# Kernel tuning notes

Hardware: AMD Instinct MI355X
Metric: run time of the kernel (lower is better)

Reference implementation:

```python
import jax, jax.numpy as jnp
import numpy as np

L = 10          # number of shooting steps
MU = 0.05       # mu hyperparameter
KS = 7          # gaussian kernel size
SIGMA = 2.0     # gaussian sigma
B, H, W = 16, 512, 512


def _conv2d(x, k, padding, groups=1):
    return jax.lax.conv_general_dilated(
        x, k, (1, 1), padding,
        dimension_numbers=('NCHW', 'OIHW', 'NCHW'),
        feature_group_count=groups)

# normalized sobel kernel (kornia SpatialGradient, abs-sum = 8)
_sobel_x = jnp.array([[-1., 0., 1.], [-2., 0., 2.], [-1., 0., 1.]], jnp.float32) / 8.0
_sobel_k = jnp.stack([_sobel_x, _sobel_x.T])[:, None]   # [2,1,3,3] -> dx, dy
_div_k = jnp.stack([_sobel_x, _sobel_x.T])[None]        # [1,2,3,3] divergence conv


def _gauss2d(ks, sigma):
    x = jnp.arange(ks, dtype=jnp.float32) - ks // 2
    g = jnp.exp(-(x ** 2) / (2.0 * sigma ** 2))
    g = g / g.sum()
    return jnp.outer(g, g)

_blur_k = jnp.broadcast_to(_gauss2d(KS, SIGMA), (2, 1, KS, KS))  # depthwise, 2 channels


def spatial_gradient(img):
    # kornia sobel SpatialGradient: replicate padding; [B,1,H,W] -> [B,1,2,H,W]
    xp = jnp.pad(img, ((0, 0), (0, 0), (1, 1), (1, 1)), mode='edge')
    g = _conv2d(xp, _sobel_k, 'VALID')  # [B,2,H,W]
    return g[:, None]


def gaussian_blur(x):
    # kornia GaussianBlur2d border_type='constant' => zero padding
    p = KS // 2
    return _conv2d(x, _blur_k, [(p, p), (p, p)], groups=2)


def div(x):
    return _conv2d(x, _div_k, [(1, 1), (1, 1)])


def grid_sample(img, grid):
    # bilinear grid_sample, pixel-coordinate grid (x,y), zero padding outside
    # img [B,C,H,W], grid [B,H,W,2]
    Bi, C, Hi, Wi = img.shape
    x, y = grid[..., 0], grid[..., 1]
    x0f, y0f = jnp.floor(x), jnp.floor(y)
    wx, wy = x - x0f, y - y0f
    x0, y0 = x0f.astype(jnp.int32), y0f.astype(jnp.int32)
    imgf = img.reshape(Bi, C, Hi * Wi)

    def gather(xi, yi):
        valid = (xi >= 0) & (xi < Wi) & (yi >= 0) & (yi < Hi)
        xc = jnp.clip(xi, 0, Wi - 1)
        yc = jnp.clip(yi, 0, Hi - 1)
        idx = (yc * Wi + xc).reshape(Bi, 1, Hi * Wi)
        v = jnp.take_along_axis(imgf, idx, axis=2).reshape(Bi, C, Hi, Wi)
        return v * valid[:, None].astype(img.dtype)

    Ia = gather(x0, y0)
    Ib = gather(x0 + 1, y0)
    Ic = gather(x0, y0 + 1)
    Id = gather(x0 + 1, y0 + 1)
    w = lambda a: a[:, None]
    return (Ia * w((1 - wx) * (1 - wy)) + Ib * w(wx * (1 - wy))
            + Ic * w((1 - wx) * wy) + Id * w(wx * wy))


def shooting(source, z0, source_seg):
    Bi, _, Hi, Wi = source.shape
    gx, gy = jnp.meshgrid(jnp.arange(Wi, dtype=source.dtype),
                          jnp.arange(Hi, dtype=source.dtype), indexing='xy')
    id_grid = jnp.stack([gx, gy], axis=-1)[None]  # [1,H,W,2] (x,y) pixel coords

    image = source
    residuals = [z0]
    phi_list = []
    mask = source_seg
    for i in range(L):
        g = spatial_gradient(image)                       # [B,1,2,H,W]
        v = gaussian_blur(-residuals[i] * g[:, 0])        # [B,2,H,W]
        f = div(residuals[i] * v) / L                     # [B,1,H,W]
        residuals.append(residuals[i] - f)
        field = jnp.transpose(v, (0, 2, 3, 1))            # [B,H,W,2]
        deformation = id_grid - field / L                 # [B,H,W,2]
        if i != 0:
            stacked = jnp.stack(phi_list)                 # [i,B,H,W,2]
            warp_phi = lambda p: jnp.transpose(
                grid_sample(jnp.transpose(p, (0, 3, 1, 2)), deformation), (0, 2, 3, 1))
            warped = jax.vmap(warp_phi)(stacked)
            phi_list = [warped[j] for j in range(i)]
        phi_list.append(deformation)
        residuals_sum = residuals[-1]
        if i > 0:
            rs = jnp.stack(residuals[1:i + 1])            # [i,B,1,H,W]
            ps = jnp.stack(phi_list[1:i + 1])             # [i,B,H,W,2]
            residuals_sum = residuals_sum + jax.vmap(grid_sample)(rs, ps).sum(0)
        mask = grid_sample(source_seg, phi_list[0])
        image = grid_sample(source, phi_list[0]) + residuals_sum * (MU ** 2 / L) * mask
    return image


def setup_inputs() -> dict:
    key = jax.random.key(0)
    k1, k2, k3 = jax.random.split(key, 3)
    source = jax.random.uniform(k1, (B, 1, H, W), jnp.float32)
    z0 = jax.random.normal(k2, (B, 1, H, W), jnp.float32) * 0.1
    source_seg = (jax.random.uniform(k3, (B, 1, H, W)) > 0.5).astype(jnp.float32)
    return {"source": source, "z0": z0, "source_seg": source_seg}


def reference(source, z0, source_seg):
    return shooting(source, z0, source_seg)
```

## Files before the change

### kernel.cpp

```cpp
#include <hip/hip_runtime.h>
#include <hip/hip_fp16.h>
#include <hip/hip_bf16.h>


namespace {
constexpr int W_ = 512, H_ = 512, L_ = 10;
constexpr int HW_ = W_ * H_;
constexpr int N_  = 16 * HW_;
constexpr float INVL = 0.1f;
constexpr float MU2L = 2.5e-4f;

typedef float f2 __attribute__((ext_vector_type(2)));

__device__ __constant__ f2 GW2[7] = {
    {0.07015933f, 0.07015933f}, {0.13107488f, 0.13107488f},
    {0.19071282f, 0.19071282f}, {0.21610594f, 0.21610594f},
    {0.19071282f, 0.19071282f}, {0.13107488f, 0.13107488f},
    {0.07015933f, 0.07015933f}};

struct BilL {
    int x0, y0;
    float w00, w01, w10, w11;
};
struct Bil {
    BilL l;
    float xc0, xc1, yc0, yc1;
};

__device__ __forceinline__ BilL mk_lite(float gx, float gy) {
    gx = fminf(fmaxf(gx, -1.0e9f), 1.0e9f);
    gy = fminf(fmaxf(gy, -1.0e9f), 1.0e9f);
    float x0f = floorf(gx), y0f = floorf(gy);
    float wx = gx - x0f, wy = gy - y0f;
    int x0 = (int)x0f, y0 = (int)y0f;
    float vx0 = ((unsigned)x0 < (unsigned)W_) ? 1.f : 0.f;
    float vx1 = ((unsigned)(x0 + 1) < (unsigned)W_) ? 1.f : 0.f;
    float vy0 = ((unsigned)y0 < (unsigned)H_) ? 1.f : 0.f;
    float vy1 = ((unsigned)(y0 + 1) < (unsigned)H_) ? 1.f : 0.f;
    BilL b;
    b.x0 = x0; b.y0 = y0;
    b.w00 = (1.f - wx) * (1.f - wy) * vx0 * vy0;
    b.w01 = wx * (1.f - wy) * vx1 * vy0;
    b.w10 = (1.f - wx) * wy * vx0 * vy1;
    b.w11 = wx * wy * vx1 * vy1;
    return b;
}

__device__ __forceinline__ Bil mk_full(float gx, float gy) {
    Bil b;
    b.l = mk_lite(gx, gy);
    int xc0 = min(max(b.l.x0, 0), W_ - 1), xc1 = min(max(b.l.x0 + 1, 0), W_ - 1);
    int yc0 = min(max(b.l.y0, 0), H_ - 1), yc1 = min(max(b.l.y0 + 1, 0), H_ - 1);
    b.xc0 = (float)xc0; b.xc1 = (float)xc1;
    b.yc0 = (float)yc0; b.yc1 = (float)yc1;
    return b;
}

__device__ __forceinline__ void gidx(const BilL& b, int& i00, int& i01,
                                     int& i10, int& i11) {
    int xc0 = min(max(b.x0, 0), W_ - 1), xc1 = min(max(b.x0 + 1, 0), W_ - 1);
    int yc0 = min(max(b.y0, 0), H_ - 1), yc1 = min(max(b.y0 + 1, 0), H_ - 1);
    i00 = yc0 * W_ + xc0; i01 = yc0 * W_ + xc1;
    i10 = yc1 * W_ + xc0; i11 = yc1 * W_ + xc1;
}

__device__ __forceinline__ float2 upk(unsigned u) {
    __half2 h; *reinterpret_cast<unsigned*>(&h) = u;
    return __half22float2(h);
}
__device__ __forceinline__ unsigned pkh(float a, float b) {
    __half2 h = __floats2half2_rn(a, b);
    return *reinterpret_cast<unsigned*>(&h);
}

__device__ __forceinline__ void warp_from(unsigned v00, unsigned v01,
                                          unsigned v10, unsigned v11,
                                          const Bil& bw, float& wxo, float& wyo) {
    float2 s00 = upk(v00), s01 = upk(v01), s10 = upk(v10), s11 = upk(v11);
    wxo = bw.l.w00 * (bw.xc0 - s00.x) + bw.l.w01 * (bw.xc1 - s01.x)
        + bw.l.w10 * (bw.xc0 - s10.x) + bw.l.w11 * (bw.xc1 - s11.x);
    wyo = bw.l.w00 * (bw.yc0 - s00.y) + bw.l.w01 * (bw.yc0 - s01.y)
        + bw.l.w10 * (bw.yc1 - s10.y) + bw.l.w11 * (bw.yc1 - s11.y);
}

__global__ __launch_bounds__(256) void k_pack2(const float* __restrict__ src,
                                               const float* __restrict__ seg,
                                               float2* __restrict__ out) {
    int idx = blockIdx.x * 256 + threadIdx.x;
    out[idx] = make_float2(src[idx], seg[idx]);
}

template <int FIRST, int WR>
__global__ __launch_bounds__(256) void k_F(const float* __restrict__ img,
                                           const float* __restrict__ rin,
                                           float* __restrict__ rnext_f,
                                           const unsigned* __restrict__ p0_old,
                                           unsigned* __restrict__ p0_new,
                                           const float* __restrict__ Bold,
                                           float* __restrict__ Bnew,
                                           const float2* __restrict__ ss2,
                                           float* __restrict__ outp) {
    __shared__ float sI[26][43];
    __shared__ float sR[24][41];
    __shared__ f2 sS2[24][41];
    __shared__ f2 sTH2[24][35];
    f2 (*sTV2)[35] = reinterpret_cast<f2 (*)[35]>(&sS2[0][0]);
    const int t = threadIdx.x;
    const int x0 = blockIdx.x * 32, y0 = blockIdx.y * 16, b = blockIdx.z;
    const size_t base = (size_t)b * HW_;
    const float* ip = img + base;
    const float* rp = rin + base;
    for (int u = t; u < 26 * 42; u += 256) {
        int r = u / 42, c = u % 42;
        int gy = min(max(y0 - 5 + r, 0), H_ - 1);
        int gx = min(max(x0 - 5 + c, 0), W_ - 1);
        sI[r][c] = ip[gy * W_ + gx];
    }
    for (int u = t; u < 24 * 40; u += 256) {
        int r = u / 40, c = u % 40;
        int gy = y0 - 4 + r, gx = x0 - 4 + c;
        sR[r][c] = ((unsigned)gy < (unsigned)H_ && (unsigned)gx < (unsigned)W_)
                 ? rp[gy * W_ + gx] : 0.f;
    }
    __syncthreads();
    if (t < 240) {
        int rq = t / 20, cq = t - rq * 20;
        int r = rq * 2, c = cq * 2;
        float a00 = sI[r][c],     a01 = sI[r][c + 1];
        float a02 = sI[r][c + 2], a03 = sI[r][c + 3];
        float a10 = sI[r + 1][c],     a11 = sI[r + 1][c + 1];
        float a12 = sI[r + 1][c + 2], a13 = sI[r + 1][c + 3];
        float a20 = sI[r + 2][c],     a21 = sI[r + 2][c + 1];
        float a22 = sI[r + 2][c + 2], a23 = sI[r + 2][c + 3];
        float a30 = sI[r + 3][c],     a31 = sI[r + 3][c + 1];
        float a32 = sI[r + 3][c + 2], a33 = sI[r + 3][c + 3];
        float rv00 = sR[r][c],     rv01 = sR[r][c + 1];
        float rv10 = sR[r + 1][c], rv11 = sR[r + 1][c + 1];
        float gx0 = ((a02 - a00) + 2.f * (a12 - a10) + (a22 - a20)) * 0.125f;
        float gy0 = ((a20 - a00) + 2.f * (a21 - a01) + (a22 - a02)) * 0.125f;
        float gx1 = ((a03 - a01) + 2.f * (a13 - a11) + (a23 - a21)) * 0.125f;
        float gy1 = ((a21 - a01) + 2.f * (a22 - a02) + (a23 - a03)) * 0.125f;
        float gx2 = ((a12 - a10) + 2.f * (a22 - a20) + (a32 - a30)) * 0.125f;
        float gy2 = ((a30 - a10) + 2.f * (a31 - a11) + (a32 - a12)) * 0.125f;
        float gx3 = ((a13 - a11) + 2.f * (a23 - a21) + (a33 - a31)) * 0.125f;
        float gy3 = ((a31 - a11) + 2.f * (a32 - a12) + (a33 - a13)) * 0.125f;
        f2 s0; s0.x = -rv00 * gx0; s0.y = -rv00 * gy0;
        f2 s1; s1.x = -rv01 * gx1; s1.y = -rv01 * gy1;
        f2 s2; s2.x = -rv10 * gx2; s2.y = -rv10 * gy2;
        f2 s3; s3.x = -rv11 * gx3; s3.y = -rv11 * gy3;
        sS2[r][c] = s0; sS2[r][c + 1] = s1;
        sS2[r + 1][c] = s2; sS2[r + 1][c + 1] = s3;
    }
    __syncthreads();
    if (t < 24 * 9) {
        int r = t / 9, q = t - (t / 9) * 9;
        int c = q * 4;
        f2 w[10];
#pragma unroll
        for (int k = 0; k < 10; k++)
            w[k] = (c + k < 40) ? sS2[r][c + k] : (f2){0.f, 0.f};
#pragma unroll
        for (int j = 0; j < 4; j++) {
            if (c + j < 34) {
                f2 a = {0.f, 0.f};
#pragma unroll
                for (int k = 0; k < 7; k++)
                    a = __builtin_elementwise_fma(GW2[k], w[j + k], a);
                sTH2[r][c + j] = a;
            }
        }
    }
    __syncthreads();
    if (t < 5 * 34) {
        int p = t / 34, c = t - (t / 34) * 34;
        int r = p * 4;
        f2 w[10];
#pragma unroll
        for (int k = 0; k < 10; k++)
            w[k] = (r + k < 24) ? sTH2[r + k][c] : (f2){0.f, 0.f};
#pragma unroll
        for (int j = 0; j < 4; j++) {
            if (r + j < 18) {
                f2 a = {0.f, 0.f};
#pragma unroll
                for (int k = 0; k < 7; k++)
                    a = __builtin_elementwise_fma(GW2[k], w[j + k], a);
                sTV2[r + j][c] = a;
            }
        }
    }
    __syncthreads();
    const int tx = t & 15, ty = t >> 4;
    const int y = y0 + ty;

    float Rp[3][4]; f2 Vp[3][4];
#pragma unroll
    for (int dy = 0; dy < 3; dy++)
#pragma unroll
        for (int dx = 0; dx < 4; dx++) {
            Rp[dy][dx] = sR[ty + 3 + dy][tx * 2 + 3 + dx];
            Vp[dy][dx] = sTV2[ty + dy][tx * 2 + dx];
        }

    float rn2[2]; unsigned ph2[2];
#pragma unroll
    for (int px = 0; px < 2; px++) {
        const int x = x0 + tx * 2 + px;
        auto Vv = [&](int ch, int dy, int dx) -> float {
            f2 v = Vp[dy + 1][px + dx + 1];
            return ch ? v.y : v.x;
        };
        auto Wt = [&](int ch, int dy, int dx) -> float {
            int yy = y + dy, xx = x + dx;
            if ((unsigned)yy >= (unsigned)H_ || (unsigned)xx >= (unsigned)W_) return 0.f;
            return Rp[dy + 1][px + dx + 1] * Vv(ch, dy, dx);
        };
        float f = (Wt(0, -1, 1) - Wt(0, -1, -1)) + 2.f * (Wt(0, 0, 1) - Wt(0, 0, -1))
                + (Wt(0, 1, 1) - Wt(0, 1, -1))
                + (Wt(1, 1, -1) - Wt(1, -1, -1)) + 2.f * (Wt(1, 1, 0) - Wt(1, -1, 0))
                + (Wt(1, 1, 1) - Wt(1, -1, 1));
        f *= 0.0125f;
        rn2[px] = Rp[1][px + 1] - f;
        ph2[px] = pkh(Vv(0, 0, 0) * INVL, Vv(1, 0, 0) * INVL);
    }
    const int idx0 = b * HW_ + y * W_ + x0 + tx * 2;
    *reinterpret_cast<float2*>(rnext_f + idx0) = make_float2(rn2[0], rn2[1]);

    const float2* ssp = ss2 + base;
    float Bv[2], ov[2]; unsigned p0w[2];
#pragma unroll
    for (int px = 0; px < 2; px++) {
        const int x = x0 + tx * 2 + px;
        float2 d = upk(ph2[px]);
        Bil bw = mk_full((float)x - d.x, (float)y - d.y);
        float Bx = rn2[px];
        BilL q = bw.l;
        if (!FIRST) {
            int i00, i01, i10, i11; gidx(bw.l, i00, i01, i10, i11);
            const unsigned* pp = p0_old + base;
            unsigned s00 = pp[i00], s01 = pp[i01], s10 = pp[i10], s11 = pp[i11];
            const float* Bp = Bold + base;
            float f00 = Bp[i00], f01 = Bp[i01], f10 = Bp[i10], f11 = Bp[i11];
            float wx, wy;
            warp_from(s00, s01, s10, s11, bw, wx, wy);
            Bx += f00 * bw.l.w00 + f01 * bw.l.w01 + f10 * bw.l.w10 + f11 * bw.l.w11;
            if (WR) p0w[px] = pkh((float)x - wx, (float)y - wy);
            q = mk_lite(wx, wy);
        } else {
            if (WR) p0w[px] = ph2[px];
        }
        int i00, i01, i10, i11; gidx(q, i00, i01, i10, i11);
        float2 c00 = ssp[i00], c01 = ssp[i01], c10 = ssp[i10], c11 = ssp[i11];
        float si = c00.x * q.w00 + c01.x * q.w01 + c10.x * q.w10 + c11.x * q.w11;
        float sg = c00.y * q.w00 + c01.y * q.w01 + c10.y * q.w10 + c11.y * q.w11;
        Bv[px] = Bx;
        ov[px] = si + Bx * MU2L * sg;
    }
    if (WR) {
        *reinterpret_cast<uint2*>(p0_new + idx0) = make_uint2(p0w[0], p0w[1]);
        *reinterpret_cast<float2*>(Bnew + idx0) = make_float2(Bv[0], Bv[1]);
    }
    *reinterpret_cast<float2*>(outp + idx0) = make_float2(ov[0], ov[1]);
}

__global__ __launch_bounds__(256) void k_copy(const float* __restrict__ a,
                                              float* __restrict__ o) {
    int idx = blockIdx.x * 256 + threadIdx.x;
    o[idx] = a[idx];
}

}

extern "C" void kernel_launch(void* const* d_in, const int* in_sizes, int n_in,
                              void* d_out, int out_size, void* d_ws, size_t ws_size,
                              hipStream_t stream) {
    const float* source = (const float*)d_in[0];
    const float* z0     = (const float*)d_in[1];
    const float* seg    = (const float*)d_in[2];
    float* out = (float*)d_out;

    const size_t UNIT = (size_t)N_ * 4;
    dim3 blk(256), g1(N_ / 256), gA(16, 32, 16);

    if (ws_size < 10 * UNIT) {
        hipLaunchKernelGGL(k_copy, g1, blk, 0, stream, source, out);
        return;
    }

    char* basep = (char*)d_ws;
    float2*   ss2    = (float2*)basep;
    float*    imgA   = (float*)(basep + 2 * UNIT);
    unsigned* phb[2] = {(unsigned*)(basep + 4 * UNIT),
                        (unsigned*)(basep + 5 * UNIT)};
    float*    Bb[2]  = {(float*)(basep + 6 * UNIT),
                        (float*)(basep + 7 * UNIT)};
    float*    rnb[2] = {(float*)(basep + 8 * UNIT),
                        (float*)(basep + 9 * UNIT)};

    hipLaunchKernelGGL(k_pack2, g1, blk, 0, stream, source, seg, ss2);

    hipLaunchKernelGGL((k_F<1, 1>), gA, blk, 0, stream,
                       source, z0, rnb[0], (const unsigned*)nullptr, phb[0],
                       (const float*)nullptr, Bb[0], (const float2*)ss2, imgA);

    for (int i = 1; i < L_; i++) {
        const float* img = (i & 1) ? imgA : out;
        float* outp      = (i & 1) ? out : imgA;
        const float* rin = rnb[(i - 1) & 1];
        float* rn_w      = rnb[i & 1];
        const unsigned* p0o = phb[(i - 1) & 1];
        unsigned* p0n       = phb[i & 1];
        const float* Bo  = Bb[(i - 1) & 1];
        float* Bn        = Bb[i & 1];
        if (i < L_ - 1)
            hipLaunchKernelGGL((k_F<0, 1>), gA, blk, 0, stream,
                               img, rin, rn_w, p0o, p0n, Bo, Bn,
                               (const float2*)ss2, outp);
        else
            hipLaunchKernelGGL((k_F<0, 0>), gA, blk, 0, stream,
                               img, rin, rn_w, p0o, p0n, Bo, Bn,
                               (const float2*)ss2, outp);
    }
    (void)in_sizes; (void)n_in; (void)out_size;
}
```

Before: 613.3 us.

## Enlarge fused step tile to 32x32 with 2x2 pixels per thread

Doubles the tile height of the fused shooting-step kernel from 16 to 32 rows, so each thread now produces a 2x2 pixel block instead of 1x2, and halves the grid in y. This cuts the share of halo work (gradient, 7x7 blur halo, divergence stencil) recomputed per output pixel. In exchange shared-memory use per block grows substantially, which can lower occupancy, and register pressure rises from the doubled per-thread state.

```diff
diff --git a/kernel.cpp b/kernel.cpp
--- a/kernel.cpp
+++ b/kernel.cpp
@@ -100,31 +100,31 @@
                                            float* __restrict__ Bnew,
                                            const float2* __restrict__ ss2,
                                            float* __restrict__ outp) {
-    __shared__ float sI[26][43];
-    __shared__ float sR[24][41];
-    __shared__ f2 sS2[24][41];
-    __shared__ f2 sTH2[24][35];
+    __shared__ float sI[42][43];
+    __shared__ float sR[40][41];
+    __shared__ f2 sS2[40][41];
+    __shared__ f2 sTH2[40][35];
     f2 (*sTV2)[35] = reinterpret_cast<f2 (*)[35]>(&sS2[0][0]);
     const int t = threadIdx.x;
-    const int x0 = blockIdx.x * 32, y0 = blockIdx.y * 16, b = blockIdx.z;
+    const int x0 = blockIdx.x * 32, y0 = blockIdx.y * 32, b = blockIdx.z;
     const size_t base = (size_t)b * HW_;
     const float* ip = img + base;
     const float* rp = rin + base;
-    for (int u = t; u < 26 * 42; u += 256) {
+    for (int u = t; u < 42 * 42; u += 256) {
         int r = u / 42, c = u % 42;
         int gy = min(max(y0 - 5 + r, 0), H_ - 1);
         int gx = min(max(x0 - 5 + c, 0), W_ - 1);
         sI[r][c] = ip[gy * W_ + gx];
     }
-    for (int u = t; u < 24 * 40; u += 256) {
+    for (int u = t; u < 40 * 40; u += 256) {
         int r = u / 40, c = u % 40;
         int gy = y0 - 4 + r, gx = x0 - 4 + c;
         sR[r][c] = ((unsigned)gy < (unsigned)H_ && (unsigned)gx < (unsigned)W_)
                  ? rp[gy * W_ + gx] : 0.f;
     }
     __syncthreads();
-    if (t < 240) {
-        int rq = t / 20, cq = t - rq * 20;
+    for (int u = t; u < 400; u += 256) {
+        int rq = u / 20, cq = u - (u / 20) * 20;
         int r = rq * 2, c = cq * 2;
         float a00 = sI[r][c],     a01 = sI[r][c + 1];
         float a02 = sI[r][c + 2], a03 = sI[r][c + 3];
@@ -152,8 +152,8 @@
         sS2[r + 1][c] = s2; sS2[r + 1][c + 1] = s3;
     }
     __syncthreads();
-    if (t < 24 * 9) {
-        int r = t / 9, q = t - (t / 9) * 9;
+    for (int u = t; u < 360; u += 256) {
+        int r = u / 9, q = u - (u / 9) * 9;
         int c = q * 4;
         f2 w[10];
 #pragma unroll
@@ -171,16 +171,16 @@
         }
     }
     __syncthreads();
-    if (t < 5 * 34) {
-        int p = t / 34, c = t - (t / 34) * 34;
+    for (int u = t; u < 306; u += 256) {
+        int p = u / 34, c = u - (u / 34) * 34;
         int r = p * 4;
         f2 w[10];
 #pragma unroll
         for (int k = 0; k < 10; k++)
-            w[k] = (r + k < 24) ? sTH2[r + k][c] : (f2){0.f, 0.f};
+            w[k] = (r + k < 40) ? sTH2[r + k][c] : (f2){0.f, 0.f};
 #pragma unroll
         for (int j = 0; j < 4; j++) {
-            if (r + j < 18) {
+            if (r + j < 34) {
                 f2 a = {0.f, 0.f};
 #pragma unroll
                 for (int k = 0; k < 7; k++)
@@ -191,49 +191,53 @@
     }
     __syncthreads();
     const int tx = t & 15, ty = t >> 4;
-    const int y = y0 + ty;
-
-    float Rp[3][4]; f2 Vp[3][4];
-#pragma unroll
-    for (int dy = 0; dy < 3; dy++)
+    const int lx0 = tx * 2, ly0 = ty * 2;
+
+    float Rp[4][4]; f2 Vp[4][4];
+#pragma unroll
+    for (int dy = 0; dy < 4; dy++)
 #pragma unroll
         for (int dx = 0; dx < 4; dx++) {
-            Rp[dy][dx] = sR[ty + 3 + dy][tx * 2 + 3 + dx];
-            Vp[dy][dx] = sTV2[ty + dy][tx * 2 + dx];
-        }
-
-    float rn2[2]; unsigned ph2[2];
+            Rp[dy][dx] = sR[ly0 + 3 + dy][lx0 + 3 + dx];
+            Vp[dy][dx] = sTV2[ly0 + dy][lx0 + dx];
+        }
+
+    float rn2[4]; unsigned ph2[4];
+#pragma unroll
+    for (int py = 0; py < 2; py++)
 #pragma unroll
     for (int px = 0; px < 2; px++) {
-        const int x = x0 + tx * 2 + px;
+        const int x = x0 + lx0 + px, y = y0 + ly0 + py;
+        const int pi = py * 2 + px;
         auto Vv = [&](int ch, int dy, int dx) -> float {
-            f2 v = Vp[dy + 1][px + dx + 1];
+            f2 v = Vp[py + dy + 1][px + dx + 1];
             return ch ? v.y : v.x;
         };
         auto Wt = [&](int ch, int dy, int dx) -> float {
             int yy = y + dy, xx = x + dx;
             if ((unsigned)yy >= (unsigned)H_ || (unsigned)xx >= (unsigned)W_) return 0.f;
-            return Rp[dy + 1][px + dx + 1] * Vv(ch, dy, dx);
+            return Rp[py + dy + 1][px + dx + 1] * Vv(ch, dy, dx);
         };
         float f = (Wt(0, -1, 1) - Wt(0, -1, -1)) + 2.f * (Wt(0, 0, 1) - Wt(0, 0, -1))
                 + (Wt(0, 1, 1) - Wt(0, 1, -1))
                 + (Wt(1, 1, -1) - Wt(1, -1, -1)) + 2.f * (Wt(1, 1, 0) - Wt(1, -1, 0))
                 + (Wt(1, 1, 1) - Wt(1, -1, 1));
         f *= 0.0125f;
-        rn2[px] = Rp[1][px + 1] - f;
-        ph2[px] = pkh(Vv(0, 0, 0) * INVL, Vv(1, 0, 0) * INVL);
-    }
-    const int idx0 = b * HW_ + y * W_ + x0 + tx * 2;
-    *reinterpret_cast<float2*>(rnext_f + idx0) = make_float2(rn2[0], rn2[1]);
+        rn2[pi] = Rp[py + 1][px + 1] - f;
+        ph2[pi] = pkh(Vv(0, 0, 0) * INVL, Vv(1, 0, 0) * INVL);
+    }
 
     const float2* ssp = ss2 + base;
-    float Bv[2], ov[2]; unsigned p0w[2];
+    float Bv[4], ov[4]; unsigned p0w[4];
+#pragma unroll
+    for (int py = 0; py < 2; py++)
 #pragma unroll
     for (int px = 0; px < 2; px++) {
-        const int x = x0 + tx * 2 + px;
-        float2 d = upk(ph2[px]);
+        const int x = x0 + lx0 + px, y = y0 + ly0 + py;
+        const int pi = py * 2 + px;
+        float2 d = upk(ph2[pi]);
         Bil bw = mk_full((float)x - d.x, (float)y - d.y);
-        float Bx = rn2[px];
+        float Bx = rn2[pi];
         BilL q = bw.l;
         if (!FIRST) {
             int i00, i01, i10, i11; gidx(bw.l, i00, i01, i10, i11);
@@ -244,23 +248,29 @@
             float wx, wy;
             warp_from(s00, s01, s10, s11, bw, wx, wy);
             Bx += f00 * bw.l.w00 + f01 * bw.l.w01 + f10 * bw.l.w10 + f11 * bw.l.w11;
-            if (WR) p0w[px] = pkh((float)x - wx, (float)y - wy);
+            if (WR) p0w[pi] = pkh((float)x - wx, (float)y - wy);
             q = mk_lite(wx, wy);
         } else {
-            if (WR) p0w[px] = ph2[px];
+            if (WR) p0w[pi] = ph2[pi];
         }
         int i00, i01, i10, i11; gidx(q, i00, i01, i10, i11);
         float2 c00 = ssp[i00], c01 = ssp[i01], c10 = ssp[i10], c11 = ssp[i11];
         float si = c00.x * q.w00 + c01.x * q.w01 + c10.x * q.w10 + c11.x * q.w11;
         float sg = c00.y * q.w00 + c01.y * q.w01 + c10.y * q.w10 + c11.y * q.w11;
-        Bv[px] = Bx;
-        ov[px] = si + Bx * MU2L * sg;
-    }
-    if (WR) {
-        *reinterpret_cast<uint2*>(p0_new + idx0) = make_uint2(p0w[0], p0w[1]);
-        *reinterpret_cast<float2*>(Bnew + idx0) = make_float2(Bv[0], Bv[1]);
-    }
-    *reinterpret_cast<float2*>(outp + idx0) = make_float2(ov[0], ov[1]);
+        Bv[pi] = Bx;
+        ov[pi] = si + Bx * MU2L * sg;
+    }
+#pragma unroll
+    for (int py = 0; py < 2; py++) {
+        const int idx0 = b * HW_ + (y0 + ly0 + py) * W_ + x0 + lx0;
+        const int pi = py * 2;
+        *reinterpret_cast<float2*>(rnext_f + idx0) = make_float2(rn2[pi], rn2[pi + 1]);
+        if (WR) {
+            *reinterpret_cast<uint2*>(p0_new + idx0) = make_uint2(p0w[pi], p0w[pi + 1]);
+            *reinterpret_cast<float2*>(Bnew + idx0) = make_float2(Bv[pi], Bv[pi + 1]);
+        }
+        *reinterpret_cast<float2*>(outp + idx0) = make_float2(ov[pi], ov[pi + 1]);
+    }
 }
 
 __global__ __launch_bounds__(256) void k_copy(const float* __restrict__ a,
@@ -280,7 +290,7 @@
     float* out = (float*)d_out;
 
     const size_t UNIT = (size_t)N_ * 4;
-    dim3 blk(256), g1(N_ / 256), gA(16, 32, 16);
+    dim3 blk(256), g1(N_ / 256), gA(16, 16, 16);
 
     if (ws_size < 10 * UNIT) {
         hipLaunchKernelGGL(k_copy, g1, blk, 0, stream, source, out);
```

Result: slower. 681.1 us (+11.1%).
